# Optimization experiments

Hardware: AMD Instinct MI355X
Metric: run time of the kernel (lower is better)

Reference implementation:

```python
import jax, jax.numpy as jnp
import numpy as np

EPS = 1e-5

def _ln(x, w, b, axes):
    mu = jnp.mean(x, axis=axes, keepdims=True)
    var = jnp.mean((x - mu) ** 2, axis=axes, keepdims=True)
    return (x - mu) / jnp.sqrt(var + EPS) * w + b

def setup_inputs() -> dict:
    key = jax.random.key(0)
    ks = jax.random.split(key, 6)
    B, L, D, A, H, F = 1, 1024, 512, 32, 8, 2048
    s = 0.02
    return {
        "x": jax.random.normal(ks[0], (B, L, D), jnp.float32),
        "ln0_w": jnp.ones((D,), jnp.float32),
        "ln0_b": jnp.zeros((D,), jnp.float32),
        "ln1_w": jnp.ones((D, H), jnp.float32),
        "ln1_b": jnp.zeros((D, H), jnp.float32),
        "qw": jax.random.normal(ks[1], (D, A * H), jnp.float32) * s,
        "qb": jnp.zeros((A * H,), jnp.float32),
        "kw": jax.random.normal(ks[2], (D, A * H), jnp.float32) * s,
        "kb": jnp.zeros((A * H,), jnp.float32),
        "vw": jax.random.normal(ks[3], (D, D * H), jnp.float32) * s,
        "vb": jnp.zeros((D * H,), jnp.float32),
        "w1": jax.random.normal(ks[4], (D * H, F), jnp.float32) * s,
        "b1": jnp.zeros((F,), jnp.float32),
        "w2": jax.random.normal(ks[5], (F, D), jnp.float32) * s,
        "b2": jnp.zeros((D,), jnp.float32),
    }

def reference(x, ln0_w, ln0_b, ln1_w, ln1_b, qw, qb, kw, kb, vw, vb, w1, b1, w2, b2):
    B, L, D = x.shape
    H = ln1_w.shape[-1]
    _x = _ln(x, ln0_w, ln0_b, -1)
    # q, k: [B, L, d_att, H] with exp(clamp(.)) feature map
    q = jnp.exp(jnp.clip(_x @ qw + qb, -10.0, 10.0)).reshape(B, L, -1, H)
    k = jnp.exp(jnp.clip(_x @ kw + kb, -10.0, 10.0)).reshape(B, L, -1, H)
    # v uses raw x (not layernormed): [B, L, D, H]
    v = (x @ vw + vb).reshape(B, L, D, H)
    # cumulative outer-product KV state: [B, L, d_att, D, H]
    kv = jnp.cumsum(jnp.einsum('blah,bldh->bladh', k, v), axis=1)
    qkv = jnp.einsum('blah,bladh->bldh', q, kv)          # [B, L, D, H]
    den = jnp.einsum('blah,blah->blh', q, jnp.cumsum(k, axis=1))[..., None, :]  # [B, L, 1, H]
    y = x[..., None] + _ln(qkv / den, ln1_w, ln1_b, (-2, -1))  # LN over (D, H) jointly
    y = y.reshape(B, L, D * H)
    h1 = jax.nn.relu(y @ w1 + b1)
    return jax.nn.relu(h1 @ w2 + b2) + x
```

## Files before the change

kernel.cpp:

```cpp
#include <hip/hip_runtime.h>
#include <hip/hip_bf16.h>
#include <math.h>

#define L_SEQ 1024
#define D_DIM 512
#define A_DIM 32
#define H_DIM 8
#define F_DIM 2048
#define AH 256
#define DH 4096
#define NC 16
#define CH 64
#define QKN 512
#define EPS_LN 1e-5f

typedef __attribute__((ext_vector_type(8))) short short8;
typedef __attribute__((ext_vector_type(4))) short short4v;
typedef __attribute__((ext_vector_type(4))) float floatx4;

#define ASYNC_COPY16(gp, lp)                                                     \
    __builtin_amdgcn_global_load_lds(                                            \
        (const __attribute__((address_space(1))) void*)(const void*)(gp),        \
        (__attribute__((address_space(3))) void*)(void*)(lp), 16, 0, 0)

__global__ __launch_bounds__(256) void prep_kernel(const float* __restrict__ x,
                                                   const float* __restrict__ ln0w,
                                                   const float* __restrict__ ln0b,
                                                   const float* __restrict__ qw,
                                                   const float* __restrict__ kw,
                                                   const float* __restrict__ vw,
                                                   const float* __restrict__ w1,
                                                   const float* __restrict__ w2,
                                                   __hip_bfloat16* __restrict__ xn,
                                                   __hip_bfloat16* __restrict__ xb,
                                                   __hip_bfloat16* __restrict__ qkwt,
                                                   __hip_bfloat16* __restrict__ vwt,
                                                   __hip_bfloat16* __restrict__ w1t,
                                                   __hip_bfloat16* __restrict__ w2t) {
    __shared__ float tt[32][33];
    __shared__ float red[8];
    int bid = blockIdx.x;
    int tid = threadIdx.x;
    if (bid < 1024) {
        int l = bid;
        float v0 = x[l * D_DIM + tid];
        float v1 = x[l * D_DIM + 256 + tid];
        float s = v0 + v1, s2 = v0 * v0 + v1 * v1;
        for (int off = 32; off > 0; off >>= 1) {
            s += __shfl_down(s, off);
            s2 += __shfl_down(s2, off);
        }
        int lane = tid & 63, wid = tid >> 6;
        if (lane == 0) { red[wid] = s; red[4 + wid] = s2; }
        __syncthreads();
        float ts = red[0] + red[1] + red[2] + red[3];
        float t2 = red[4] + red[5] + red[6] + red[7];
        float mu = ts / (float)D_DIM;
        float var = t2 / (float)D_DIM - mu * mu;
        float rs = rsqrtf(var + EPS_LN);
        xn[l * D_DIM + tid]       = (__hip_bfloat16)((v0 - mu) * rs * ln0w[tid] + ln0b[tid]);
        xn[l * D_DIM + 256 + tid] = (__hip_bfloat16)((v1 - mu) * rs * ln0w[256 + tid] + ln0b[256 + tid]);
        xb[l * D_DIM + tid]       = (__hip_bfloat16)v0;
        xb[l * D_DIM + 256 + tid] = (__hip_bfloat16)v1;
        return;
    }
    const float* in;
    __hip_bfloat16* out;
    int R, C, mode = 0, t;
    if (bid < 1152)      { t = bid - 1024;  in = qw; out = qkwt;                      R = 512;  C = 256; }
    else if (bid < 1280) { t = bid - 1152;  in = kw; out = qkwt + (size_t)AH * D_DIM; R = 512;  C = 256; }
    else if (bid < 3328) { t = bid - 1280;  in = vw; out = vwt;  mode = 1;            R = 512;  C = 4096; }
    else if (bid < 11520){ t = bid - 3328;  in = w1; out = w1t;                       R = 4096; C = 2048; }
    else                 { t = bid - 11520; in = w2; out = w2t;                       R = 2048; C = 512; }
    int ctiles = C >> 5;
    int cx = t % ctiles, cy = t / ctiles;
    int tx = tid & 31, ti = tid >> 5;
    int r0 = cy * 32, c0 = cx * 32;
#pragma unroll
    for (int ii = 0; ii < 4; ++ii)
        tt[ti + ii * 8][tx] = in[(size_t)(r0 + ti + ii * 8) * C + c0 + tx];
    __syncthreads();
#pragma unroll
    for (int ii = 0; ii < 4; ++ii) {
        int c = c0 + ti + ii * 8;
        int orow = mode ? (((c & 7) << 9) | (c >> 3)) : c;
        out[(size_t)orow * R + r0 + tx] = (__hip_bfloat16)tt[tx][ti + ii * 8];
    }
}

__device__ __forceinline__ void gemm_core(const __hip_bfloat16* __restrict__ A,
                                          const __hip_bfloat16* __restrict__ Bt,
                                          int K, int bm, int bn, int k_beg, int k_end,
                                          __hip_bfloat16* As, __hip_bfloat16* Bs,
                                          floatx4 acc[2][2]) {
    const int tid = threadIdx.x;
    const int w = tid >> 6, lane = tid & 63;
    const int wm = (w >> 1) * 32, wn = (w & 1) * 32;
    const int quad = lane >> 4, l16 = lane & 15;
    const int srow = tid >> 4, sslot = tid & 15;
    const int scg = sslot ^ srow;
    for (int k0 = k_beg; k0 < k_end; k0 += 128) {
        __syncthreads();
#pragma unroll
        for (int j = 0; j < 4; ++j) {
            ASYNC_COPY16(A + (size_t)(bm + j * 16 + srow) * K + k0 + scg * 8,
                         As + j * 2048 + w * 512);
            ASYNC_COPY16(Bt + (size_t)(bn + j * 16 + srow) * K + k0 + scg * 8,
                         Bs + j * 2048 + w * 512);
        }
        __syncthreads();
#pragma unroll
        for (int ks = 0; ks < 4; ++ks) {
            short8 af[2], bfr[2];
#pragma unroll
            for (int mt = 0; mt < 2; ++mt) {
                int rr = wm + mt * 16 + l16;
                af[mt] = *(const short8*)(As + rr * 128 + (((ks * 4 + quad) ^ (rr & 15)) * 8));
            }
#pragma unroll
            for (int nt = 0; nt < 2; ++nt) {
                int rr = wn + nt * 16 + l16;
                bfr[nt] = *(const short8*)(Bs + rr * 128 + (((ks * 4 + quad) ^ (rr & 15)) * 8));
            }
#pragma unroll
            for (int mt = 0; mt < 2; ++mt)
#pragma unroll
                for (int nt = 0; nt < 2; ++nt)
                    acc[mt][nt] = __builtin_amdgcn_mfma_f32_16x16x32_bf16(
                        af[mt], bfr[nt], acc[mt][nt], 0, 0, 0);
        }
    }
}

__global__ __launch_bounds__(256) void qkv_gemm(const __hip_bfloat16* __restrict__ xn,
                                                const __hip_bfloat16* __restrict__ xb,
                                                const __hip_bfloat16* __restrict__ qkwt,
                                                const __hip_bfloat16* __restrict__ vwt,
                                                const float* __restrict__ qb,
                                                const float* __restrict__ kb,
                                                const float* __restrict__ vb,
                                                float* __restrict__ qk,
                                                __hip_bfloat16* __restrict__ vT) {
    __shared__ __align__(16) __hip_bfloat16 As[64 * 128];
    __shared__ __align__(16) __hip_bfloat16 Bs[64 * 128];
    const int tid = threadIdx.x;
    const int w = tid >> 6, lane = tid & 63;
    const int wm = (w >> 1) * 32, wn = (w & 1) * 32;
    const int quad = lane >> 4, l16 = lane & 15;
    int bid = blockIdx.x;
    bool isv = bid < 1024;
    const __hip_bfloat16 *A, *Bt;
    int bx, by;
    if (isv) {
        int r = bid >> 3;
        bx = (bid & 7) * 8 + (r & 7);
        by = r >> 3;
        A = xb; Bt = vwt;
    } else {
        int b2 = bid - 1024;
        bx = b2 & 7; by = b2 >> 3;
        A = xn; Bt = qkwt;
    }
    const int bm = by * 64, bn = bx * 64;
    floatx4 acc[2][2];
#pragma unroll
    for (int i = 0; i < 2; ++i)
#pragma unroll
        for (int j = 0; j < 2; ++j) acc[i][j] = (floatx4)0.f;
    gemm_core(A, Bt, D_DIM, bm, bn, 0, D_DIM, As, Bs, acc);
    if (isv) {
        __syncthreads();
        __hip_bfloat16* Ct = As;
#pragma unroll
        for (int mt = 0; mt < 2; ++mt)
#pragma unroll
            for (int nt = 0; nt < 2; ++nt) {
                int col = bn + wn + nt * 16 + l16;
                int bi = ((col & 511) << 3) | (col >> 9);
                float bbv = vb[bi];
                __hip_bfloat16 tmp[4];
#pragma unroll
                for (int r = 0; r < 4; ++r)
                    tmp[r] = (__hip_bfloat16)(acc[mt][nt][r] + bbv);
                *(short4v*)&Ct[(wn + nt * 16 + l16) * 72 + wm + mt * 16 + quad * 4] =
                    *(short4v*)tmp;
            }
        __syncthreads();
        int colloc = tid >> 2, seg = (tid & 3) * 16;
        short8 o0 = *(const short8*)&Ct[colloc * 72 + seg];
        short8 o1 = *(const short8*)&Ct[colloc * 72 + seg + 8];
        *(short8*)(vT + (size_t)(bn + colloc) * 1024 + bm + seg) = o0;
        *(short8*)(vT + (size_t)(bn + colloc) * 1024 + bm + seg + 8) = o1;
    } else {
#pragma unroll
        for (int mt = 0; mt < 2; ++mt)
#pragma unroll
            for (int nt = 0; nt < 2; ++nt)
#pragma unroll
                for (int r = 0; r < 4; ++r) {
                    int row = bm + wm + mt * 16 + quad * 4 + r;
                    int col = bn + wn + nt * 16 + l16;
                    float bb = (col < 256) ? qb[col] : kb[col - 256];
                    qk[(size_t)row * QKN + col] =
                        expf(fminf(fmaxf(acc[mt][nt][r] + bb, -10.f), 10.f));
                }
    }
}

template <int STRIP>
__global__ __launch_bounds__(256) void gemm_split(const __hip_bfloat16* __restrict__ A,
                                                  const __hip_bfloat16* __restrict__ Bt,
                                                  float* __restrict__ part,
                                                  int M, int N, int K, int Ksub) {
    __shared__ __align__(16) __hip_bfloat16 As[64 * 128];
    __shared__ __align__(16) __hip_bfloat16 Bs[64 * 128];
    const int tid = threadIdx.x;
    const int w = tid >> 6, lane = tid & 63;
    const int wm = (w >> 1) * 32, wn = (w & 1) * 32;
    const int quad = lane >> 4, l16 = lane & 15;
    int bid = blockIdx.x;
    int r = bid >> 3;
    int bx = (bid & 7) * STRIP + (r % STRIP);
    int by = r / STRIP;
    const int bm = by * 64, bn = bx * 64;
    const int kz = blockIdx.z;
    floatx4 acc[2][2];
#pragma unroll
    for (int i = 0; i < 2; ++i)
#pragma unroll
        for (int j = 0; j < 2; ++j) acc[i][j] = (floatx4)0.f;
    gemm_core(A, Bt, K, bm, bn, kz * Ksub, kz * Ksub + Ksub, As, Bs, acc);
#pragma unroll
    for (int mt = 0; mt < 2; ++mt)
#pragma unroll
        for (int nt = 0; nt < 2; ++nt)
#pragma unroll
            for (int rr = 0; rr < 4; ++rr) {
                int row = bm + wm + mt * 16 + quad * 4 + rr;
                int col = bn + wn + nt * 16 + l16;
                part[((size_t)kz * M + row) * N + col] = acc[mt][nt][rr];
            }
}

__global__ __launch_bounds__(256) void w1red(const float* __restrict__ part,
                                             const float* __restrict__ b1,
                                             __hip_bfloat16* __restrict__ h1) {
    size_t e = ((size_t)blockIdx.x * 256 + threadIdx.x) * 4;
    const size_t MN = (size_t)L_SEQ * F_DIM;
    float4 p0 = *(const float4*)(part + e);
    float4 p1 = *(const float4*)(part + MN + e);
    float4 bb = *(const float4*)(b1 + (e & (F_DIM - 1)));
    h1[e + 0] = (__hip_bfloat16)fmaxf(p0.x + p1.x + bb.x, 0.f);
    h1[e + 1] = (__hip_bfloat16)fmaxf(p0.y + p1.y + bb.y, 0.f);
    h1[e + 2] = (__hip_bfloat16)fmaxf(p0.z + p1.z + bb.z, 0.f);
    h1[e + 3] = (__hip_bfloat16)fmaxf(p0.w + p1.w + bb.w, 0.f);
}

__global__ __launch_bounds__(256) void w2red(const float* __restrict__ part,
                                             const float* __restrict__ b2,
                                             const float* __restrict__ x,
                                             float* __restrict__ out) {
    size_t e = ((size_t)blockIdx.x * 256 + threadIdx.x) * 4;
    const size_t MN = (size_t)L_SEQ * D_DIM;
    float4 v0 = *(const float4*)(part + e);
    float4 v1 = *(const float4*)(part + MN + e);
    float4 v2 = *(const float4*)(part + 2 * MN + e);
    float4 v3 = *(const float4*)(part + 3 * MN + e);
    float4 bb = *(const float4*)(b2 + (e & 511));
    float4 xx = *(const float4*)(x + e);
    float4 r;
    r.x = fmaxf(v0.x + v1.x + v2.x + v3.x + bb.x, 0.f) + xx.x;
    r.y = fmaxf(v0.y + v1.y + v2.y + v3.y + bb.y, 0.f) + xx.y;
    r.z = fmaxf(v0.z + v1.z + v2.z + v3.z + bb.z, 0.f) + xx.z;
    r.w = fmaxf(v0.w + v1.w + v2.w + v3.w + bb.w, 0.f) + xx.w;
    *(float4*)(out + e) = r;
}

__global__ __launch_bounds__(256) void kvchunk_kernel(const float* __restrict__ qk,
                                                      const __hip_bfloat16* __restrict__ vT,
                                                      float* __restrict__ S,
                                                      float* __restrict__ Ka) {
    int c = blockIdx.x, h = blockIdx.y, dq = blockIdx.z;
    int tid = threadIdx.x;
    __shared__ __align__(16) __hip_bfloat16 kaT[32][72];
    __shared__ __align__(16) float St[128][36];
    for (int e = tid; e < 2048; e += 256) {
        int l = e >> 5, a = e & 31;
        kaT[a][l] = (__hip_bfloat16)qk[(c * CH + l) * QKN + 256 + a * 8 + h];
    }
    __syncthreads();
    int w = tid >> 6, lane = tid & 63, quad = lane >> 4, l16 = lane & 15;
    floatx4 acc[2][2];
#pragma unroll
    for (int i = 0; i < 2; ++i)
#pragma unroll
        for (int j = 0; j < 2; ++j) acc[i][j] = (floatx4)0.f;
#pragma unroll
    for (int ks = 0; ks < 2; ++ks) {
        short8 af[2], bfr[2];
#pragma unroll
        for (int mt = 0; mt < 2; ++mt)
            af[mt] = *(const short8*)&kaT[mt * 16 + l16][ks * 32 + quad * 8];
#pragma unroll
        for (int nt = 0; nt < 2; ++nt)
            bfr[nt] = *(const short8*)(vT + (size_t)(h * 512 + dq * 128 + w * 32 + nt * 16 + l16) * 1024
                                       + c * 64 + ks * 32 + quad * 8);
#pragma unroll
        for (int mt = 0; mt < 2; ++mt)
#pragma unroll
            for (int nt = 0; nt < 2; ++nt)
                acc[mt][nt] = __builtin_amdgcn_mfma_f32_16x16x32_bf16(
                    af[mt], bfr[nt], acc[mt][nt], 0, 0, 0);
    }
#pragma unroll
    for (int mt = 0; mt < 2; ++mt)
#pragma unroll
        for (int nt = 0; nt < 2; ++nt)
            *(floatx4*)&St[w * 32 + nt * 16 + l16][mt * 16 + quad * 4] = acc[mt][nt];
    __syncthreads();
    int d = tid >> 1, aseg = (tid & 1) * 16;
    float* dst = S + (size_t)((c * 8 + h) * 512 + dq * 128 + d) * 32 + aseg;
    const float* src = &St[d][aseg];
#pragma unroll
    for (int j = 0; j < 4; ++j)
        *(float4*)(dst + j * 4) = *(const float4*)(src + j * 4);
    if (dq == 0 && tid < 32) {
        float s = 0.f;
        for (int l = 0; l < CH; ++l) s += (float)kaT[tid][l];
        Ka[c * AH + tid * 8 + h] = s;
    }
}

__global__ __launch_bounds__(256) void scan_kernel(const float* __restrict__ S,
                                                   const float* __restrict__ Ka,
                                                   __hip_bfloat16* __restrict__ P2,
                                                   float* __restrict__ KaP) {
    size_t j = ((size_t)blockIdx.x * 256 + threadIdx.x) * 4;
    const size_t CS = 8 * 512 * 32;
    float4 run = {0.f, 0.f, 0.f, 0.f};
    for (int c = 0; c < NC; ++c) {
        __hip_bfloat16 o[4] = {(__hip_bfloat16)run.x, (__hip_bfloat16)run.y,
                               (__hip_bfloat16)run.z, (__hip_bfloat16)run.w};
        *(short4v*)&P2[c * CS + j] = *(short4v*)o;
        float4 sv = *(const float4*)(S + c * CS + j);
        run.x += sv.x; run.y += sv.y; run.z += sv.z; run.w += sv.w;
    }
    if (blockIdx.x == 0) {
        int t = threadIdx.x;
        float rk = 0.f;
        for (int c = 0; c < NC; ++c) {
            KaP[c * AH + t] = rk;
            rk += Ka[c * AH + t];
        }
    }
}

__global__ __launch_bounds__(256) void passC_kernel(const float* __restrict__ qk,
                                                    const __hip_bfloat16* __restrict__ vT,
                                                    const __hip_bfloat16* __restrict__ P2,
                                                    const float* __restrict__ KaP,
                                                    __hip_bfloat16* __restrict__ qkv,
                                                    float* __restrict__ den) {
    int c = blockIdx.x, h = blockIdx.y, dq = blockIdx.z;
    int tid = threadIdx.x;
    __shared__ __align__(16) __hip_bfloat16 qa[64][40];
    __shared__ __align__(16) __hip_bfloat16 ka[64][40];
    __shared__ __align__(16) __hip_bfloat16 Sc[64][72];
    __shared__ float KaPs[32];
    for (int e = tid; e < 2048; e += 256) {
        int l = e >> 5, a = e & 31;
        int gi = (c * CH + l) * QKN + a * 8 + h;
        qa[l][a] = (__hip_bfloat16)qk[gi];
        ka[l][a] = (__hip_bfloat16)qk[gi + 256];
    }
    if (dq == 0 && tid < 32) KaPs[tid] = KaP[c * AH + tid * 8 + h];
    __syncthreads();
    int w = tid >> 6, lane = tid & 63, quad = lane >> 4, l16 = lane & 15;
    short8 afq = *(const short8*)&qa[w * 16 + l16][quad * 8];
    floatx4 sacc[4];
#pragma unroll
    for (int nt = 0; nt < 4; ++nt) sacc[nt] = (floatx4)0.f;
#pragma unroll
    for (int nt = 0; nt < 4; ++nt) {
        short8 bfr = *(const short8*)&ka[nt * 16 + l16][quad * 8];
        sacc[nt] = __builtin_amdgcn_mfma_f32_16x16x32_bf16(afq, bfr, sacc[nt], 0, 0, 0);
    }
#pragma unroll
    for (int nt = 0; nt < 4; ++nt)
#pragma unroll
        for (int r = 0; r < 4; ++r) {
            int l = w * 16 + quad * 4 + r;
            int lp = nt * 16 + l16;
            Sc[l][lp] = (__hip_bfloat16)((lp <= l) ? sacc[nt][r] : 0.f);
        }
    __syncthreads();
    if (dq == 0 && tid < 64) {
        int l = tid;
        float s = 0.f;
        for (int lp = 0; lp <= l; ++lp) s += (float)Sc[l][lp];
        for (int a = 0; a < A_DIM; ++a) s += (float)qa[l][a] * KaPs[a];
        den[(c * CH + l) * H_DIM + h] = s;
    }
    floatx4 acc[8];
#pragma unroll
    for (int nt = 0; nt < 8; ++nt) acc[nt] = (floatx4)0.f;
#pragma unroll
    for (int nt = 0; nt < 8; ++nt) {
        short8 pb = *(const short8*)(P2 + ((size_t)((c * 8 + h) * 512 + dq * 128 + nt * 16 + l16)) * 32 + quad * 8);
        acc[nt] = __builtin_amdgcn_mfma_f32_16x16x32_bf16(afq, pb, acc[nt], 0, 0, 0);
    }
#pragma unroll
    for (int ks = 0; ks < 2; ++ks) {
        short8 afs = *(const short8*)&Sc[w * 16 + l16][ks * 32 + quad * 8];
#pragma unroll
        for (int nt = 0; nt < 8; ++nt) {
            short8 bfr = *(const short8*)(vT + (size_t)(h * 512 + dq * 128 + nt * 16 + l16) * 1024
                                          + c * 64 + ks * 32 + quad * 8);
            acc[nt] = __builtin_amdgcn_mfma_f32_16x16x32_bf16(afs, bfr, acc[nt], 0, 0, 0);
        }
    }
#pragma unroll
    for (int nt = 0; nt < 8; ++nt)
#pragma unroll
        for (int r = 0; r < 4; ++r) {
            int l = w * 16 + quad * 4 + r;
            int d = dq * 128 + nt * 16 + l16;
            qkv[(size_t)(c * CH + l) * DH + h * D_DIM + d] = (__hip_bfloat16)acc[nt][r];
        }
}

__global__ __launch_bounds__(256) void ln1_kernel(const __hip_bfloat16* __restrict__ qkv,
                                                  const float* __restrict__ den,
                                                  const float* __restrict__ x,
                                                  const float* __restrict__ w,
                                                  const float* __restrict__ b,
                                                  __hip_bfloat16* __restrict__ y) {
    int l = blockIdx.x, tid = threadIdx.x;
    __shared__ float dsh[8];
    __shared__ float yl[DH];
    __shared__ float red[8];
    if (tid < 8) dsh[tid] = den[l * H_DIM + tid];
    __syncthreads();
    float t[16];
    float s = 0.f, s2 = 0.f;
#pragma unroll
    for (int j = 0; j < 16; ++j) {
        int e = j * 256 + tid;
        float val = (float)qkv[(size_t)l * DH + e] / dsh[e >> 9];
        t[j] = val;
        s += val;
        s2 += val * val;
    }
    for (int off = 32; off > 0; off >>= 1) {
        s += __shfl_down(s, off);
        s2 += __shfl_down(s2, off);
    }
    int lane = tid & 63, wid = tid >> 6;
    if (lane == 0) { red[wid] = s; red[4 + wid] = s2; }
    __syncthreads();
    float ts = red[0] + red[1] + red[2] + red[3];
    float t2 = red[4] + red[5] + red[6] + red[7];
    float mu = ts / (float)DH;
    float var = t2 / (float)DH - mu * mu;
    float rs = rsqrtf(var + EPS_LN);
#pragma unroll
    for (int j = 0; j < 16; ++j) {
        int e = j * 256 + tid;
        int h = e >> 9, d = e & 511;
        int dh = d * H_DIM + h;
        yl[dh] = x[l * D_DIM + d] + (t[j] - mu) * rs * w[dh] + b[dh];
    }
    __syncthreads();
#pragma unroll
    for (int j = 0; j < 16; ++j) {
        int e = j * 256 + tid;
        y[(size_t)l * DH + e] = (__hip_bfloat16)yl[e];
    }
}

extern "C" void kernel_launch(void* const* d_in, const int* in_sizes, int n_in,
                              void* d_out, int out_size, void* d_ws, size_t ws_size,
                              hipStream_t stream) {
    const float* x     = (const float*)d_in[0];
    const float* ln0_w = (const float*)d_in[1];
    const float* ln0_b = (const float*)d_in[2];
    const float* ln1_w = (const float*)d_in[3];
    const float* ln1_b = (const float*)d_in[4];
    const float* qw    = (const float*)d_in[5];
    const float* qb    = (const float*)d_in[6];
    const float* kw    = (const float*)d_in[7];
    const float* kb    = (const float*)d_in[8];
    const float* vw    = (const float*)d_in[9];
    const float* vb    = (const float*)d_in[10];
    const float* w1    = (const float*)d_in[11];
    const float* b1    = (const float*)d_in[12];
    const float* w2    = (const float*)d_in[13];
    const float* b2    = (const float*)d_in[14];
    float* out = (float*)d_out;

    char* ws = (char*)d_ws;
    __hip_bfloat16* xn_bf = (__hip_bfloat16*)(ws + 0);
    __hip_bfloat16* xbf   = (__hip_bfloat16*)(ws + 1048576);
    __hip_bfloat16* qkwt  = (__hip_bfloat16*)(ws + 2097152);
    __hip_bfloat16* vwt   = (__hip_bfloat16*)(ws + 2621440);
    __hip_bfloat16* w1t   = (__hip_bfloat16*)(ws + 6815744);
    __hip_bfloat16* w2t   = (__hip_bfloat16*)(ws + 23592960);
    float* qk  = (float*)(ws + 25690112);
    __hip_bfloat16* vT = (__hip_bfloat16*)(ws + 27787264);
    float* S   = (float*)(ws + 36175872);
    __hip_bfloat16* P2 = (__hip_bfloat16*)(ws + 44564480);
    __hip_bfloat16* qkvb = (__hip_bfloat16*)(ws + 52953088);
    float* Ka  = (float*)(ws + 61341696);
    float* den = (float*)(ws + 61358080);
    float* KaP = (float*)(ws + 61390848);
    float* w1part = (float*)(ws + 61440000);
    __hip_bfloat16* y  = (__hip_bfloat16*)(ws + 44564480);
    __hip_bfloat16* h1 = (__hip_bfloat16*)S;
    float* w2part = (float*)qkvb;

    prep_kernel<<<12544, 256, 0, stream>>>(x, ln0_w, ln0_b, qw, kw, vw, w1, w2,
                                           xn_bf, xbf, qkwt, vwt, w1t, w2t);
    qkv_gemm<<<1152, 256, 0, stream>>>(xn_bf, xbf, qkwt, vwt, qb, kb, vb, qk, vT);
    kvchunk_kernel<<<dim3(NC, H_DIM, 4), 256, 0, stream>>>(qk, vT, S, Ka);
    scan_kernel<<<128, 256, 0, stream>>>(S, Ka, P2, KaP);
    passC_kernel<<<dim3(NC, H_DIM, 4), 256, 0, stream>>>(qk, vT, P2, KaP, qkvb, den);
    ln1_kernel<<<L_SEQ, 256, 0, stream>>>(qkvb, den, x, ln1_w, ln1_b, y);
    gemm_split<4><<<dim3(512, 1, 2), 256, 0, stream>>>(y, w1t, w1part,
                                                       L_SEQ, F_DIM, DH, DH / 2);
    w1red<<<(L_SEQ * F_DIM) / 1024, 256, 0, stream>>>(w1part, b1, h1);
    gemm_split<1><<<dim3(128, 1, 4), 256, 0, stream>>>(h1, w2t, w2part,
                                                       L_SEQ, D_DIM, F_DIM, F_DIM / 4);
    w2red<<<(L_SEQ * D_DIM) / 1024, 256, 0, stream>>>(w2part, b2, x, out);

    (void)in_sizes; (void)n_in; (void)out_size; (void)ws_size;
}
```

Before: 213.3 us.

## Store q/k as head-major bf16 and permute ln1/w1 layout to vectorize ln1

The qkv GEMM epilogue now writes q and k as bf16 in a per-head [H][L][A] layout, staged through shared memory, instead of an fp32 interleaved buffer. kvchunk and passC can then load contiguous 16-byte vectors, and passC reads its MFMA fragments straight from global memory rather than staging them in shared memory. The ln1 weights and biases and the w1 rows are permuted once in prep so that ln1 can process a contiguous head-major slice per thread with vector loads and stores, without the shared-memory scatter. This halves q/k traffic and removes gathers. In exchange it adds an extra block to prep and a permuted read of w1 during its transpose.

After: 206.2 us. 3.3% less time.

```diff
diff --git a/kernel.cpp b/kernel.cpp
--- a/kernel.cpp
+++ b/kernel.cpp
@@ -11,7 +11,6 @@
 #define DH 4096
 #define NC 16
 #define CH 64
-#define QKN 512
 #define EPS_LN 1e-5f
 
 typedef __attribute__((ext_vector_type(8))) short short8;
@@ -26,6 +25,8 @@
 __global__ __launch_bounds__(256) void prep_kernel(const float* __restrict__ x,
                                                    const float* __restrict__ ln0w,
                                                    const float* __restrict__ ln0b,
+                                                   const float* __restrict__ ln1w,
+                                                   const float* __restrict__ ln1b,
                                                    const float* __restrict__ qw,
                                                    const float* __restrict__ kw,
                                                    const float* __restrict__ vw,
@@ -36,7 +37,9 @@
                                                    __hip_bfloat16* __restrict__ qkwt,
                                                    __hip_bfloat16* __restrict__ vwt,
                                                    __hip_bfloat16* __restrict__ w1t,
-                                                   __hip_bfloat16* __restrict__ w2t) {
+                                                   __hip_bfloat16* __restrict__ w2t,
+                                                   float* __restrict__ wp,
+                                                   float* __restrict__ bp) {
     __shared__ float tt[32][33];
     __shared__ float red[8];
     int bid = blockIdx.x;
@@ -64,26 +67,46 @@
         xb[l * D_DIM + 256 + tid] = (__hip_bfloat16)v1;
         return;
     }
+    if (bid == 12544) {
+        int e0 = tid * 16;
+        float o1[16], o2[16];
+#pragma unroll
+        for (int j = 0; j < 16; ++j) {
+            int ee = e0 + j;
+            int pi = ((ee & 511) << 3) | (ee >> 9);
+            o1[j] = ln1w[pi];
+            o2[j] = ln1b[pi];
+        }
+#pragma unroll
+        for (int j = 0; j < 4; ++j) {
+            *(float4*)(wp + e0 + j * 4) = *(float4*)&o1[j * 4];
+            *(float4*)(bp + e0 + j * 4) = *(float4*)&o2[j * 4];
+        }
+        return;
+    }
     const float* in;
     __hip_bfloat16* out;
     int R, C, mode = 0, t;
     if (bid < 1152)      { t = bid - 1024;  in = qw; out = qkwt;                      R = 512;  C = 256; }
     else if (bid < 1280) { t = bid - 1152;  in = kw; out = qkwt + (size_t)AH * D_DIM; R = 512;  C = 256; }
     else if (bid < 3328) { t = bid - 1280;  in = vw; out = vwt;  mode = 1;            R = 512;  C = 4096; }
-    else if (bid < 11520){ t = bid - 3328;  in = w1; out = w1t;                       R = 4096; C = 2048; }
+    else if (bid < 11520){ t = bid - 3328;  in = w1; out = w1t;  mode = 2;            R = 4096; C = 2048; }
     else                 { t = bid - 11520; in = w2; out = w2t;                       R = 2048; C = 512; }
     int ctiles = C >> 5;
     int cx = t % ctiles, cy = t / ctiles;
     int tx = tid & 31, ti = tid >> 5;
     int r0 = cy * 32, c0 = cx * 32;
 #pragma unroll
-    for (int ii = 0; ii < 4; ++ii)
-        tt[ti + ii * 8][tx] = in[(size_t)(r0 + ti + ii * 8) * C + c0 + tx];
+    for (int ii = 0; ii < 4; ++ii) {
+        int rr = r0 + ti + ii * 8;
+        if (mode == 2) rr = ((rr & 511) << 3) | (rr >> 9);
+        tt[ti + ii * 8][tx] = in[(size_t)rr * C + c0 + tx];
+    }
     __syncthreads();
 #pragma unroll
     for (int ii = 0; ii < 4; ++ii) {
         int c = c0 + ti + ii * 8;
-        int orow = mode ? (((c & 7) << 9) | (c >> 3)) : c;
+        int orow = (mode == 1) ? (((c & 7) << 9) | (c >> 3)) : c;
         out[(size_t)orow * R + r0 + tx] = (__hip_bfloat16)tt[tx][ti + ii * 8];
     }
 }
@@ -139,7 +162,8 @@
                                                 const float* __restrict__ qb,
                                                 const float* __restrict__ kb,
                                                 const float* __restrict__ vb,
-                                                float* __restrict__ qk,
+                                                __hip_bfloat16* __restrict__ q2,
+                                                __hip_bfloat16* __restrict__ k2,
                                                 __hip_bfloat16* __restrict__ vT) {
     __shared__ __align__(16) __hip_bfloat16 As[64 * 128];
     __shared__ __align__(16) __hip_bfloat16 Bs[64 * 128];
@@ -192,18 +216,35 @@
         *(short8*)(vT + (size_t)(bn + colloc) * 1024 + bm + seg) = o0;
         *(short8*)(vT + (size_t)(bn + colloc) * 1024 + bm + seg + 8) = o1;
     } else {
+        __syncthreads();
+        __hip_bfloat16* q2t = As;
+        bool isq = bn < 256;
+        const float* bias = isq ? qb : kb;
+        int cb = isq ? bn : bn - 256;
 #pragma unroll
         for (int mt = 0; mt < 2; ++mt)
 #pragma unroll
-            for (int nt = 0; nt < 2; ++nt)
+            for (int nt = 0; nt < 2; ++nt) {
+                int colloc = wn + nt * 16 + l16;
+                float bb = bias[cb + colloc];
+                int hh = colloc & 7, aa = colloc >> 3;
 #pragma unroll
                 for (int r = 0; r < 4; ++r) {
-                    int row = bm + wm + mt * 16 + quad * 4 + r;
-                    int col = bn + wn + nt * 16 + l16;
-                    float bb = (col < 256) ? qb[col] : kb[col - 256];
-                    qk[(size_t)row * QKN + col] =
-                        expf(fminf(fmaxf(acc[mt][nt][r] + bb, -10.f), 10.f));
+                    int rowloc = wm + mt * 16 + quad * 4 + r;
+                    float val = expf(fminf(fmaxf(acc[mt][nt][r] + bb, -10.f), 10.f));
+                    q2t[((hh * 64 + rowloc) << 3) + aa] = (__hip_bfloat16)val;
                 }
+            }
+        __syncthreads();
+        __hip_bfloat16* dst = isq ? q2 : k2;
+        int a0 = cb >> 3;
+#pragma unroll
+        for (int j = 0; j < 2; ++j) {
+            int p = tid + j * 256;
+            int hh = p >> 6, ll = p & 63;
+            short8 o = *(const short8*)&q2t[(hh * 64 + ll) << 3];
+            *(short8*)(dst + (size_t)(hh * 1024 + bm + ll) * 32 + a0) = o;
+        }
     }
 }
 
@@ -276,7 +317,7 @@
     *(float4*)(out + e) = r;
 }
 
-__global__ __launch_bounds__(256) void kvchunk_kernel(const float* __restrict__ qk,
+__global__ __launch_bounds__(256) void kvchunk_kernel(const __hip_bfloat16* __restrict__ k2,
                                                       const __hip_bfloat16* __restrict__ vT,
                                                       float* __restrict__ S,
                                                       float* __restrict__ Ka) {
@@ -284,9 +325,12 @@
     int tid = threadIdx.x;
     __shared__ __align__(16) __hip_bfloat16 kaT[32][72];
     __shared__ __align__(16) float St[128][36];
-    for (int e = tid; e < 2048; e += 256) {
-        int l = e >> 5, a = e & 31;
-        kaT[a][l] = (__hip_bfloat16)qk[(c * CH + l) * QKN + 256 + a * 8 + h];
+    {
+        int l = tid >> 2, a0s = (tid & 3) * 8;
+        short8 kv8 = *(const short8*)(k2 + (size_t)(h * 1024 + c * 64 + l) * 32 + a0s);
+#pragma unroll
+        for (int j = 0; j < 8; ++j)
+            kaT[a0s + j][l] = ((const __hip_bfloat16*)&kv8)[j];
     }
     __syncthreads();
     int w = tid >> 6, lane = tid & 63, quad = lane >> 4, l16 = lane & 15;
@@ -355,7 +399,8 @@
     }
 }
 
-__global__ __launch_bounds__(256) void passC_kernel(const float* __restrict__ qk,
+__global__ __launch_bounds__(256) void passC_kernel(const __hip_bfloat16* __restrict__ q2,
+                                                    const __hip_bfloat16* __restrict__ k2,
                                                     const __hip_bfloat16* __restrict__ vT,
                                                     const __hip_bfloat16* __restrict__ P2,
                                                     const float* __restrict__ KaP,
@@ -363,26 +408,18 @@
                                                     float* __restrict__ den) {
     int c = blockIdx.x, h = blockIdx.y, dq = blockIdx.z;
     int tid = threadIdx.x;
-    __shared__ __align__(16) __hip_bfloat16 qa[64][40];
-    __shared__ __align__(16) __hip_bfloat16 ka[64][40];
     __shared__ __align__(16) __hip_bfloat16 Sc[64][72];
     __shared__ float KaPs[32];
-    for (int e = tid; e < 2048; e += 256) {
-        int l = e >> 5, a = e & 31;
-        int gi = (c * CH + l) * QKN + a * 8 + h;
-        qa[l][a] = (__hip_bfloat16)qk[gi];
-        ka[l][a] = (__hip_bfloat16)qk[gi + 256];
-    }
     if (dq == 0 && tid < 32) KaPs[tid] = KaP[c * AH + tid * 8 + h];
-    __syncthreads();
     int w = tid >> 6, lane = tid & 63, quad = lane >> 4, l16 = lane & 15;
-    short8 afq = *(const short8*)&qa[w * 16 + l16][quad * 8];
+    const size_t qbase = (size_t)(h * 1024 + c * 64) * 32;
+    short8 afq = *(const short8*)(q2 + qbase + (w * 16 + l16) * 32 + quad * 8);
     floatx4 sacc[4];
 #pragma unroll
     for (int nt = 0; nt < 4; ++nt) sacc[nt] = (floatx4)0.f;
 #pragma unroll
     for (int nt = 0; nt < 4; ++nt) {
-        short8 bfr = *(const short8*)&ka[nt * 16 + l16][quad * 8];
+        short8 bfr = *(const short8*)(k2 + qbase + (nt * 16 + l16) * 32 + quad * 8);
         sacc[nt] = __builtin_amdgcn_mfma_f32_16x16x32_bf16(afq, bfr, sacc[nt], 0, 0, 0);
     }
 #pragma unroll
@@ -398,7 +435,8 @@
         int l = tid;
         float s = 0.f;
         for (int lp = 0; lp <= l; ++lp) s += (float)Sc[l][lp];
-        for (int a = 0; a < A_DIM; ++a) s += (float)qa[l][a] * KaPs[a];
+        const __hip_bfloat16* qp = q2 + qbase + l * 32;
+        for (int a = 0; a < A_DIM; ++a) s += (float)qp[a] * KaPs[a];
         den[(c * CH + l) * H_DIM + h] = s;
     }
     floatx4 acc[8];
@@ -432,25 +470,26 @@
 __global__ __launch_bounds__(256) void ln1_kernel(const __hip_bfloat16* __restrict__ qkv,
                                                   const float* __restrict__ den,
                                                   const float* __restrict__ x,
-                                                  const float* __restrict__ w,
-                                                  const float* __restrict__ b,
+                                                  const float* __restrict__ wp,
+                                                  const float* __restrict__ bp,
                                                   __hip_bfloat16* __restrict__ y) {
     int l = blockIdx.x, tid = threadIdx.x;
-    __shared__ float dsh[8];
-    __shared__ float yl[DH];
     __shared__ float red[8];
-    if (tid < 8) dsh[tid] = den[l * H_DIM + tid];
-    __syncthreads();
-    float t[16];
+    int h = tid >> 5;
+    int e0 = tid * 16;
+    int d0 = e0 & 511;
+    float rden = 1.f / den[l * 8 + h];
+    short8 v0 = *(const short8*)(qkv + (size_t)l * DH + e0);
+    short8 v1 = *(const short8*)(qkv + (size_t)l * DH + e0 + 8);
+    float vals[16];
     float s = 0.f, s2 = 0.f;
 #pragma unroll
-    for (int j = 0; j < 16; ++j) {
-        int e = j * 256 + tid;
-        float val = (float)qkv[(size_t)l * DH + e] / dsh[e >> 9];
-        t[j] = val;
-        s += val;
-        s2 += val * val;
-    }
+    for (int j = 0; j < 8; ++j) {
+        vals[j] = (float)((const __hip_bfloat16*)&v0)[j] * rden;
+        vals[8 + j] = (float)((const __hip_bfloat16*)&v1)[j] * rden;
+    }
+#pragma unroll
+    for (int j = 0; j < 16; ++j) { s += vals[j]; s2 += vals[j] * vals[j]; }
     for (int off = 32; off > 0; off >>= 1) {
         s += __shfl_down(s, off);
         s2 += __shfl_down(s2, off);
@@ -463,19 +502,19 @@
     float mu = ts / (float)DH;
     float var = t2 / (float)DH - mu * mu;
     float rs = rsqrtf(var + EPS_LN);
-#pragma unroll
-    for (int j = 0; j < 16; ++j) {
-        int e = j * 256 + tid;
-        int h = e >> 9, d = e & 511;
-        int dh = d * H_DIM + h;
-        yl[dh] = x[l * D_DIM + d] + (t[j] - mu) * rs * w[dh] + b[dh];
-    }
-    __syncthreads();
-#pragma unroll
-    for (int j = 0; j < 16; ++j) {
-        int e = j * 256 + tid;
-        y[(size_t)l * DH + e] = (__hip_bfloat16)yl[e];
-    }
+    __hip_bfloat16 o[16];
+#pragma unroll
+    for (int j4 = 0; j4 < 4; ++j4) {
+        float4 xx = *(const float4*)(x + l * D_DIM + d0 + j4 * 4);
+        float4 wv = *(const float4*)(wp + e0 + j4 * 4);
+        float4 bv = *(const float4*)(bp + e0 + j4 * 4);
+        o[j4 * 4 + 0] = (__hip_bfloat16)(xx.x + (vals[j4 * 4 + 0] - mu) * rs * wv.x + bv.x);
+        o[j4 * 4 + 1] = (__hip_bfloat16)(xx.y + (vals[j4 * 4 + 1] - mu) * rs * wv.y + bv.y);
+        o[j4 * 4 + 2] = (__hip_bfloat16)(xx.z + (vals[j4 * 4 + 2] - mu) * rs * wv.z + bv.z);
+        o[j4 * 4 + 3] = (__hip_bfloat16)(xx.w + (vals[j4 * 4 + 3] - mu) * rs * wv.w + bv.w);
+    }
+    *(short8*)(y + (size_t)l * DH + e0) = *(short8*)&o[0];
+    *(short8*)(y + (size_t)l * DH + e0 + 8) = *(short8*)&o[8];
 }
 
 extern "C" void kernel_launch(void* const* d_in, const int* in_sizes, int n_in,
@@ -505,26 +544,30 @@
     __hip_bfloat16* vwt   = (__hip_bfloat16*)(ws + 2621440);
     __hip_bfloat16* w1t   = (__hip_bfloat16*)(ws + 6815744);
     __hip_bfloat16* w2t   = (__hip_bfloat16*)(ws + 23592960);
-    float* qk  = (float*)(ws + 25690112);
-    __hip_bfloat16* vT = (__hip_bfloat16*)(ws + 27787264);
-    float* S   = (float*)(ws + 36175872);
-    __hip_bfloat16* P2 = (__hip_bfloat16*)(ws + 44564480);
-    __hip_bfloat16* qkvb = (__hip_bfloat16*)(ws + 52953088);
-    float* Ka  = (float*)(ws + 61341696);
-    float* den = (float*)(ws + 61358080);
-    float* KaP = (float*)(ws + 61390848);
-    float* w1part = (float*)(ws + 61440000);
-    __hip_bfloat16* y  = (__hip_bfloat16*)(ws + 44564480);
+    __hip_bfloat16* q2    = (__hip_bfloat16*)(ws + 25690112);
+    __hip_bfloat16* k2    = (__hip_bfloat16*)(ws + 26214400);
+    __hip_bfloat16* vT    = (__hip_bfloat16*)(ws + 26738688);
+    float* S              = (float*)(ws + 35127296);
+    __hip_bfloat16* P2    = (__hip_bfloat16*)(ws + 43515904);
+    __hip_bfloat16* qkvb  = (__hip_bfloat16*)(ws + 51904512);
+    float* Ka  = (float*)(ws + 60293120);
+    float* KaP = (float*)(ws + 60309504);
+    float* den = (float*)(ws + 60325888);
+    float* wp  = (float*)(ws + 60358656);
+    float* bp  = (float*)(ws + 60375040);
+    float* w1part = (float*)(ws + 60391424);
+    __hip_bfloat16* y  = P2;
     __hip_bfloat16* h1 = (__hip_bfloat16*)S;
     float* w2part = (float*)qkvb;
 
-    prep_kernel<<<12544, 256, 0, stream>>>(x, ln0_w, ln0_b, qw, kw, vw, w1, w2,
-                                           xn_bf, xbf, qkwt, vwt, w1t, w2t);
-    qkv_gemm<<<1152, 256, 0, stream>>>(xn_bf, xbf, qkwt, vwt, qb, kb, vb, qk, vT);
-    kvchunk_kernel<<<dim3(NC, H_DIM, 4), 256, 0, stream>>>(qk, vT, S, Ka);
+    prep_kernel<<<12545, 256, 0, stream>>>(x, ln0_w, ln0_b, ln1_w, ln1_b,
+                                           qw, kw, vw, w1, w2,
+                                           xn_bf, xbf, qkwt, vwt, w1t, w2t, wp, bp);
+    qkv_gemm<<<1152, 256, 0, stream>>>(xn_bf, xbf, qkwt, vwt, qb, kb, vb, q2, k2, vT);
+    kvchunk_kernel<<<dim3(NC, H_DIM, 4), 256, 0, stream>>>(k2, vT, S, Ka);
     scan_kernel<<<128, 256, 0, stream>>>(S, Ka, P2, KaP);
-    passC_kernel<<<dim3(NC, H_DIM, 4), 256, 0, stream>>>(qk, vT, P2, KaP, qkvb, den);
-    ln1_kernel<<<L_SEQ, 256, 0, stream>>>(qkvb, den, x, ln1_w, ln1_b, y);
+    passC_kernel<<<dim3(NC, H_DIM, 4), 256, 0, stream>>>(q2, k2, vT, P2, KaP, qkvb, den);
+    ln1_kernel<<<L_SEQ, 256, 0, stream>>>(qkvb, den, x, wp, bp, y);
     gemm_split<4><<<dim3(512, 1, 2), 256, 0, stream>>>(y, w1t, w1part,
                                                        L_SEQ, F_DIM, DH, DH / 2);
     w1red<<<(L_SEQ * F_DIM) / 1024, 256, 0, stream>>>(w1part, b1, h1);
```
